# Optimization experiments

Measured on AMD Instinct MI355X. Metric: run time of the kernel, lower is better.

Reference implementation:

```python
import jax, jax.numpy as jnp
import numpy as np

B, L, D = 2, 4096, 768   # batch, seq_len, in_dim
BN = 384                 # bottleneck = in_dim / reduction_rate(2)
DI = 768                 # d_inner = expand(2) * bottleneck
NS = 16                  # d_state
DC = 4                   # d_conv
R  = 24                  # dt_rank = ceil(bottleneck / 16)


def _ln(x, g, b):
    m = x.mean(-1, keepdims=True)
    v = ((x - m) ** 2).mean(-1, keepdims=True)
    return (x - m) / jnp.sqrt(v + 1e-5) * g + b


def _mamba(x, in_W, conv_w, conv_b, xproj_W, dt_W, dt_b, A_log, Dp, out_W):
    # x: (B, L, BN)
    Bb, Ll, _ = x.shape
    xz = x @ in_W                                  # (B, L, 2*DI)
    xs, z = jnp.split(xz, 2, axis=-1)
    # causal depthwise conv over time
    xc = jnp.transpose(xs, (0, 2, 1))              # (B, DI, L)
    xc = jax.lax.conv_general_dilated(
        xc, conv_w[:, None, :], (1,), [(DC - 1, 0)],
        dimension_numbers=('NCH', 'OIH', 'NCH'), feature_group_count=DI)
    xc = jax.nn.silu(xc + conv_b[None, :, None])
    u = jnp.transpose(xc, (0, 2, 1))               # (B, L, DI)
    x_dbl = u @ xproj_W                            # (B, L, R + 2*NS)
    dt, Bm, Cm = jnp.split(x_dbl, [R, R + NS], axis=-1)
    dt = jax.nn.softplus(dt @ dt_W + dt_b)         # (B, L, DI)
    A = -jnp.exp(A_log)                            # (DI, NS)

    def step(h, inp):
        dt_t, B_t, C_t, u_t = inp                  # (B,DI),(B,NS),(B,NS),(B,DI)
        dA = jnp.exp(dt_t[:, :, None] * A)         # (B, DI, NS)
        h = dA * h + (dt_t * u_t)[:, :, None] * B_t[:, None, :]
        y = (h * C_t[:, None, :]).sum(-1)          # (B, DI)
        return h, y

    tm = lambda a: jnp.transpose(a, (1, 0, 2))     # time-major
    h0 = jnp.zeros((Bb, DI, NS), x.dtype)
    _, ys = jax.lax.scan(step, h0, (tm(dt), tm(Bm), tm(Cm), tm(u)))
    y = jnp.transpose(ys, (1, 0, 2)) + u * Dp      # (B, L, DI)
    y = y * jax.nn.silu(z)
    return y @ out_W                               # (B, L, BN)


def setup_inputs() -> dict:
    key = jax.random.key(0)
    ks = jax.random.split(key, 32)
    n = lambda i, shape, s=0.02: jax.random.normal(ks[i], shape, jnp.float32) * s
    inp = {
        'x': jax.random.normal(ks[0], (B, L, D), jnp.float32),
        'down_W': n(1, (D, BN)), 'down_b': jnp.zeros((BN,), jnp.float32),
        'up_W': n(2, (BN, D)), 'up_b': jnp.zeros((D,), jnp.float32),
    }
    A_log = jnp.log(jnp.tile(jnp.arange(1, NS + 1, dtype=jnp.float32), (DI, 1)))
    for pi, p in enumerate(['f', 'b']):
        o = 3 + pi * 10
        inp[p + '_in_W'] = n(o, (BN, 2 * DI))
        inp[p + '_conv_w'] = n(o + 1, (DI, DC), 0.1)
        inp[p + '_conv_b'] = jnp.zeros((DI,), jnp.float32)
        inp[p + '_xproj_W'] = n(o + 2, (DI, R + 2 * NS))
        inp[p + '_dt_W'] = n(o + 3, (R, DI), 0.1)
        inp[p + '_dt_b'] = n(o + 4, (DI,), 0.5)
        inp[p + '_A_log'] = A_log
        inp[p + '_D'] = jnp.ones((DI,), jnp.float32)
        inp[p + '_out_W'] = n(o + 5, (DI, BN))
        inp[p + '_ln_g'] = jnp.ones((BN,), jnp.float32)
        inp[p + '_ln_b'] = jnp.zeros((BN,), jnp.float32)
    return inp


def reference(x, down_W, down_b, up_W, up_b,
              f_in_W, f_conv_w, f_conv_b, f_xproj_W, f_dt_W, f_dt_b, f_A_log, f_D, f_out_W, f_ln_g, f_ln_b,
              b_in_W, b_conv_w, b_conv_b, b_xproj_W, b_dt_W, b_dt_b, b_A_log, b_D, b_out_W, b_ln_g, b_ln_b):
    h = x @ down_W + down_b                        # (B, L, BN)
    fwd = _ln(_mamba(h, f_in_W, f_conv_w, f_conv_b, f_xproj_W, f_dt_W, f_dt_b,
                     f_A_log, f_D, f_out_W), f_ln_g, f_ln_b)
    bwd = _ln(_mamba(h[:, ::-1], b_in_W, b_conv_w, b_conv_b, b_xproj_W, b_dt_W, b_dt_b,
                     b_A_log, b_D, b_out_W), b_ln_g, b_ln_b)
    y = fwd + bwd[:, ::-1]
    return y @ up_W + up_b
```

## Files before the change

### kernel.cpp

```cpp
#include <hip/hip_runtime.h>

typedef short bf16x8 __attribute__((ext_vector_type(8)));
typedef float f32x4 __attribute__((ext_vector_type(4)));
typedef float f32x2 __attribute__((ext_vector_type(2)));
typedef unsigned int u32x4 __attribute__((ext_vector_type(4)));

constexpr int Bq  = 2;
constexpr int Lq  = 4096;
constexpr int BNq = 384;
constexpr int DIq = 768;
constexpr int NSq = 16;
constexpr int Rq  = 24;
constexpr int XDq = 56;
constexpr int XLD = 64;
constexpr int CSq = 32;
constexpr int NCq = Lq / CSq;

__device__ __forceinline__ float b2f(unsigned short u) {
    unsigned int x = ((unsigned int)u) << 16;
    return __builtin_bit_cast(float, x);
}
__device__ __forceinline__ unsigned short f2b(float f) {
    unsigned int x = __builtin_bit_cast(unsigned int, f);
    return (unsigned short)((x + 0x8000u) >> 16);
}
__device__ __forceinline__ f32x2 bfpair(unsigned int v) {
    f32x2 r;
    r[0] = __builtin_bit_cast(float, v << 16);
    r[1] = __builtin_bit_cast(float, v & 0xFFFF0000u);
    return r;
}
__device__ __forceinline__ float softplus_fast(float v) {
    float e = __expf(-fabsf(v));
    return fmaxf(v, 0.f) + __logf(1.f + e);
}

typedef const __attribute__((address_space(1))) void gvoid_t;
typedef __attribute__((address_space(3))) void svoid_t;
__device__ __forceinline__ void gload_lds16(const void* g, void* l) {
    __builtin_amdgcn_global_load_lds((gvoid_t*)g, (svoid_t*)l, 16, 0, 0);
}

__device__ __forceinline__ void vm_wait(int n) {
    if (n <= 0)      asm volatile("s_waitcnt vmcnt(0)" ::: "memory");
    else if (n == 1) asm volatile("s_waitcnt vmcnt(1)" ::: "memory");
    else if (n == 2) asm volatile("s_waitcnt vmcnt(2)" ::: "memory");
    else if (n == 3) asm volatile("s_waitcnt vmcnt(3)" ::: "memory");
    else if (n == 4) asm volatile("s_waitcnt vmcnt(4)" ::: "memory");
    else if (n == 5) asm volatile("s_waitcnt vmcnt(5)" ::: "memory");
    else if (n == 6) asm volatile("s_waitcnt vmcnt(6)" ::: "memory");
    else if (n == 7) asm volatile("s_waitcnt vmcnt(6)" ::: "memory");
    else             asm volatile("s_waitcnt vmcnt(8)" ::: "memory");
}

__global__ __launch_bounds__(256) void cast_k(
    const float* __restrict__ src, unsigned short* __restrict__ dst, int n4)
{
    int i = blockIdx.x * 256 + threadIdx.x;
    if (i >= n4) return;
    f32x4 v = *(const f32x4*)(src + (size_t)i * 4);
    unsigned short o[4];
#pragma unroll
    for (int k = 0; k < 4; ++k) o[k] = f2b(v[k]);
    *(unsigned long long*)(dst + (size_t)i * 4) = *(unsigned long long*)o;
}

template<int BM, int BN, int WM, int WN, int TM, int TN, int NBUF, bool SWZ = false, int MINW = 2>
__global__ __launch_bounds__(WM * WN * 64, MINW) void gemm_t(
    const unsigned short* __restrict__ Ag, int lda, long sA,
    const unsigned short* __restrict__ Wg, long sW,
    const float* __restrict__ bias0, const float* __restrict__ bias1,
    void* __restrict__ Cg, int ldc, long sC,
    int Nn, int Kk, int epi)
{
    constexpr int NW   = WM * WN;
    constexpr int HALF = (BM + BN) * 32;
    constexpr int RT   = TM * 16;
    constexpr int CT   = TN * 16;
    constexpr int EPSH = RT * CT;
    constexpr int SMSZ = (NBUF * HALF > NW * EPSH) ? NBUF * HALF : NW * EPSH;
    __shared__ __align__(16) unsigned short Sm[SMSZ];

    const int z = blockIdx.z;
    const unsigned short* A = Ag + (size_t)z * sA;
    const unsigned short* W = Wg + (size_t)z * sW;
    const float* bias = z ? bias1 : bias0;

    int bx = blockIdx.x, by = blockIdx.y;
    if (SWZ) {
        int gx = gridDim.x, gy = gridDim.y;
        int stripe = bx & 7;
        int idx = (bx >> 3) + (gx >> 3) * by;
        int lin = stripe * ((gx >> 3) * gy) + idx;
        bx = lin / gy; by = lin % gy;
    }
    const int m0   = bx * BM;
    const int n0   = by * BN;

    const int tid  = threadIdx.x;
    const int lane = tid & 63;
    const int wid  = tid >> 6;
    const int row0 = (wid % WM) * RT;
    const int col0 = (wid / WM) * CT;
    const int lrow = lane & 15;
    const int lq   = lane >> 4;
    const int sub  = lane & 15;
    const int q    = lane >> 4;

    constexpr int NRG = (BM + BN) / 16;
    static_assert(NRG % NW == 0, "need uniform loads per wave for vmcnt counting");
    constexpr int NG = NRG / NW;
    constexpr int D  = NBUF - 1;

    const unsigned short* gbase[NG];
    {
        int ng = 0;
        for (int rg = wid; rg < NRG; rg += NW, ++ng) {
            if (rg * 16 < BM) gbase[ng] = A + (size_t)(m0 + rg * 16 + sub) * lda + q * 8;
            else              gbase[ng] = W + (size_t)(n0 + (rg * 16 - BM) + sub) * Kk + q * 8;
        }
    }
    auto stage = [&](int buf, int k0) {
        int ng = 0;
        for (int rg = wid; rg < NRG; rg += NW, ++ng)
            gload_lds16(gbase[ng] + k0, &Sm[buf * HALF + rg * 512]);
    };

    f32x4 zero4 = {0.f, 0.f, 0.f, 0.f};
    f32x4 acc[TM][TN];
#pragma unroll
    for (int i = 0; i < TM; ++i)
#pragma unroll
        for (int j = 0; j < TN; ++j) acc[i][j] = zero4;

    const int nsteps = Kk >> 5;
    for (int i = 0; i < D && i < nsteps; ++i) stage(i, i * 32);

    int buf = 0;
    for (int k = 0; k < nsteps; ++k) {
        int rem = nsteps - (k + 1);
        vm_wait((rem < D - 1 ? rem : D - 1) * NG);
        __builtin_amdgcn_s_barrier();
        asm volatile("" ::: "memory");

        if (k + D < nsteps) {
            int wb = buf + D; if (wb >= NBUF) wb -= NBUF;
            stage(wb, (k + D) * 32);
        }

        const unsigned short* As = &Sm[buf * HALF];
        const unsigned short* Bs = As + BM * 32;
        bf16x8 af[TM], bfv[TN];
#pragma unroll
        for (int i = 0; i < TM; ++i)
            af[i] = *(const bf16x8*)(&As[((row0 >> 4) + i) * 512 + lq * 128 + lrow * 8]);
#pragma unroll
        for (int j = 0; j < TN; ++j)
            bfv[j] = *(const bf16x8*)(&Bs[((col0 >> 4) + j) * 512 + lq * 128 + lrow * 8]);
#pragma unroll
        for (int i = 0; i < TM; ++i)
#pragma unroll
            for (int j = 0; j < TN; ++j)
                acc[i][j] = __builtin_amdgcn_mfma_f32_16x16x32_bf16(af[i], bfv[j], acc[i][j], 0, 0, 0);
        if (++buf == NBUF) buf = 0;
    }

    if (epi == 3) {
#pragma unroll
        for (int j = 0; j < TN; ++j) {
            int col = n0 + col0 + j * 16 + lrow;
            if (col >= Nn) continue;
            float bv = bias ? bias[col] : 0.f;
#pragma unroll
            for (int i = 0; i < TM; ++i)
#pragma unroll
                for (int r = 0; r < 4; ++r) {
                    int rowm = m0 + row0 + i * 16 + lq * 4 + r;
                    ((float*)Cg)[(size_t)z * sC + (size_t)rowm * ldc + col] = acc[i][j][r] + bv;
                }
        }
    } else {
        __syncthreads();
        unsigned short* Ep = Sm + wid * EPSH;
#pragma unroll
        for (int j = 0; j < TN; ++j) {
            int col = n0 + col0 + j * 16 + lrow;
            float bv = bias ? bias[col] : 0.f;
#pragma unroll
            for (int i = 0; i < TM; ++i)
#pragma unroll
                for (int r = 0; r < 4; ++r) {
                    float v = acc[i][j][r] + bv;
                    if (epi == 2) v = softplus_fast(v);
                    Ep[(i * 16 + lq * 4 + r) * CT + j * 16 + lrow] = f2b(v);
                }
        }
#pragma unroll
        for (int e = 0; e < EPSH / 512; ++e) {
            int ei = e * 512 + lane * 8;
            int lr = ei / CT, lc = ei % CT;
            int gr = m0 + row0 + lr, gc = n0 + col0 + lc;
            if (gc < Nn) {
                bf16x8 v = *(const bf16x8*)(&Ep[lr * CT + lc]);
                *(bf16x8*)((unsigned short*)Cg + (size_t)z * sC + (size_t)gr * ldc + gc) = v;
            }
        }
    }
}

__global__ __launch_bounds__(256) void conv_silu_k(
    const unsigned short* __restrict__ xz,
    const float* __restrict__ cwf, const float* __restrict__ cbf,
    const float* __restrict__ cwb, const float* __restrict__ cbb,
    unsigned short* __restrict__ u)
{
    int idx = blockIdx.x * 256 + threadIdx.x;
    int dir = blockIdx.y;
    int row = idx / 96;
    int c   = (idx - row * 96) * 8;
    int bb = row >> 12, tt = row & (Lq - 1);

    const float* cw = dir ? cwb : cwf;
    const float* cb = dir ? cbb : cbf;

    f32x4 w[8];
#pragma unroll
    for (int e = 0; e < 8; ++e) w[e] = *(const f32x4*)(cw + (c + e) * 4);
    f32x4 b0 = *(const f32x4*)(cb + c);
    f32x4 b1 = *(const f32x4*)(cb + c + 4);

    float acc[8];
#pragma unroll
    for (int e = 0; e < 4; ++e) { acc[e] = b0[e]; acc[4 + e] = b1[e]; }

#pragma unroll
    for (int j = 0; j < 4; ++j) {
        int ts = dir ? (tt + j) : (tt - 3 + j);
        int widx = dir ? (3 - j) : j;
        if (ts >= 0 && ts < Lq) {
            bf16x8 xv = *(const bf16x8*)(xz + (size_t)((bb << 12) + ts) * 3072 + dir * 1536 + c);
#pragma unroll
            for (int e = 0; e < 8; ++e)
                acc[e] += w[e][widx] * b2f(((unsigned short*)&xv)[e]);
        }
    }

    unsigned short o[8];
#pragma unroll
    for (int e = 0; e < 8; ++e) {
        float s = acc[e] / (1.f + __expf(-acc[e]));
        o[e] = f2b(s);
    }
    *(bf16x8*)(u + ((size_t)dir * 8192 + row) * DIq + c) = *(bf16x8*)o;
}

__device__ __forceinline__ void gp_ladder(float g1, f32x2 (&gp2)[8]) {
    float g2 = g1 * g1;
    gp2[0][0] = g1; gp2[0][1] = g2;
    f32x2 e2; e2[0] = g2; e2[1] = g2;
    gp2[1] = gp2[0] * e2;
    f32x2 e4; e4[0] = gp2[1][1]; e4[1] = gp2[1][1];
    gp2[2] = gp2[0] * e4;
    gp2[3] = gp2[1] * e4;
    f32x2 e8; e8[0] = gp2[3][1]; e8[1] = gp2[3][1];
#pragma unroll
    for (int k = 0; k < 4; ++k) gp2[4 + k] = gp2[k] * e8;
}

template<int DIR>
__device__ __forceinline__ void scan_p1_impl(
    const unsigned short* __restrict__ dt,
    const unsigned short* __restrict__ u,
    const unsigned short* __restrict__ xdbl,
    float* __restrict__ S, float* __restrict__ sumdt,
    int chunk, int cb3, int bb)
{
    const int ch = cb3 * 256 + threadIdx.x;
    const size_t rowbase = (size_t)DIR * 8192 + (bb << 12) + chunk * CSq;

    constexpr int sgn = DIR ? -1 : 1;
    constexpr int tt0 = DIR ? (CSq - 1) : 0;
    constexpr int PF  = 4;
    constexpr int NGR = CSq / PF;
    static_assert(CSq % PF == 0, "pf");

    const unsigned short* pd = dt + (rowbase + tt0) * DIq + ch;
    const unsigned short* pu = u  + (rowbase + tt0) * DIq + ch;
    const u32x4* prow = (const u32x4*)(xdbl + (rowbase + tt0) * XLD + Rq);

    f32x2 h2[8];
#pragma unroll
    for (int k = 0; k < 8; ++k) { h2[k][0] = 0.f; h2[k][1] = 0.f; }
    float sdt = 0.f;

    unsigned short db_[PF], ub_[PF];
#pragma unroll
    for (int i = 0; i < PF; ++i) {
        db_[i] = *pd; ub_[i] = *pu;
        pd += sgn * DIq; pu += sgn * DIq;
    }
    u32x4 q0 = prow[0], q1 = prow[1];

    auto body = [&](unsigned short dv16, unsigned short uv16,
                    const u32x4& a0, const u32x4& a1) {
        float dtv = b2f(dv16);
        float uv  = b2f(uv16);
        float du  = dtv * uv;
        sdt += dtv;
        f32x2 du2; du2[0] = du; du2[1] = du;
        f32x2 gp2[8];
        gp_ladder(__expf(-dtv), gp2);
        unsigned int w[8] = {a0[0], a0[1], a0[2], a0[3], a1[0], a1[1], a1[2], a1[3]};
#pragma unroll
        for (int k = 0; k < 8; ++k)
            h2[k] = h2[k] * gp2[k] + du2 * bfpair(w[k]);
    };

#pragma unroll 1
    for (int g = 0; g < NGR - 1; ++g) {
#pragma unroll
        for (int i = 0; i < PF; ++i) {
            unsigned short dv = db_[i], uv = ub_[i];
            db_[i] = *pd; ub_[i] = *pu;
            pd += sgn * DIq; pu += sgn * DIq;
            prow += sgn * 8;
            u32x4 n0 = prow[0], n1 = prow[1];
            body(dv, uv, q0, q1);
            q0 = n0; q1 = n1;
        }
    }
#pragma unroll
    for (int i = 0; i < PF; ++i) {
        unsigned short dv = db_[i], uv = ub_[i];
        if (i < PF - 1) {
            prow += sgn * 8;
            u32x4 n0 = prow[0], n1 = prow[1];
            body(dv, uv, q0, q1);
            q0 = n0; q1 = n1;
        } else {
            body(dv, uv, q0, q1);
        }
    }

    size_t base = (((size_t)DIR * Bq + bb) * NCq + chunk) * DIq + ch;
    sumdt[base] = sdt;
    f32x4* Sp = (f32x4*)(S + base * 16);
#pragma unroll
    for (int q4 = 0; q4 < 4; ++q4) {
        f32x4 t;
        t[0] = h2[2 * q4][0]; t[1] = h2[2 * q4][1];
        t[2] = h2[2 * q4 + 1][0]; t[3] = h2[2 * q4 + 1][1];
        Sp[q4] = t;
    }
}

__global__ __launch_bounds__(256) void scan_p1_k(
    const unsigned short* __restrict__ dt,
    const unsigned short* __restrict__ u,
    const unsigned short* __restrict__ xdbl,
    float* __restrict__ S, float* __restrict__ sumdt)
{
    int dir = blockIdx.z >> 1, bb = blockIdx.z & 1;
    if (dir == 0) scan_p1_impl<0>(dt, u, xdbl, S, sumdt, blockIdx.x, blockIdx.y, bb);
    else          scan_p1_impl<1>(dt, u, xdbl, S, sumdt, blockIdx.x, blockIdx.y, bb);
}

__global__ __launch_bounds__(256) void scan_p2_k(
    const float* __restrict__ sumdt,
    float* __restrict__ S)
{
    int idx = blockIdx.x * 256 + threadIdx.x;
    int ss = idx & 15;
    int rest = idx >> 4;
    int ch = rest % DIq;
    int db = rest / DIq;
    int dir = db >> 1;
    float Av = -(float)(ss + 1);

    constexpr int TB = 16;
    constexpr int NT = NCq / TB;
    static_assert(NCq % TB == 0, "tile");

    auto baseOf = [&](int i) {
        int c = dir ? (NCq - 1 - i) : i;
        return ((size_t)db * NCq + c) * DIq + ch;
    };

    float svA[TB], sdA[TB], svB[TB], sdB[TB];

    auto loadT = [&](int t, float (&sv)[TB], float (&sd)[TB]) {
#pragma unroll
        for (int i = 0; i < TB; ++i) {
            size_t b = baseOf(t * TB + i);
            sv[i] = S[b * 16 + ss];
            sd[i] = sumdt[b];
        }
    };

    float h = 0.f;
    auto chainT = [&](int t, const float (&sv)[TB], const float (&sd)[TB]) {
#pragma unroll
        for (int i = 0; i < TB; ++i) {
            size_t b = baseOf(t * TB + i);
            S[b * 16 + ss] = h;
            h = h * __expf(Av * sd[i]) + sv[i];
        }
    };

    loadT(0, svA, sdA);
#pragma unroll
    for (int t = 0; t < NT; t += 2) {
        if (t + 1 < NT) loadT(t + 1, svB, sdB);
        chainT(t, svA, sdA);
        if (t + 2 < NT) loadT(t + 2, svA, sdA);
        if (t + 1 < NT) chainT(t + 1, svB, sdB);
    }
}

template<int DIR>
__device__ __forceinline__ void scan_p3_impl(
    const unsigned short* __restrict__ dt,
    const unsigned short* __restrict__ u,
    const unsigned short* __restrict__ xdbl,
    unsigned short* __restrict__ xz,
    const float* __restrict__ Dp,
    const float* __restrict__ Hin,
    int chunk, int cb3, int bb)
{
    const int ch = cb3 * 256 + threadIdx.x;
    const size_t rowbase = (size_t)DIR * 8192 + (bb << 12) + chunk * CSq;
    const float Dv = Dp[ch];

    constexpr int sgn = DIR ? -1 : 1;
    constexpr int tt0 = DIR ? (CSq - 1) : 0;
    constexpr int PF  = 4;
    constexpr int NGR = CSq / PF;
    static_assert(CSq % PF == 0, "pf");
    const size_t lbase = (size_t)(bb << 12) + chunk * CSq;

    const unsigned short* pd = dt + (rowbase + tt0) * DIq + ch;
    const unsigned short* pu = u  + (rowbase + tt0) * DIq + ch;
    const unsigned short* pz = xz + (lbase + tt0) * 3072 + DIR * 1536 + 768 + ch;
    unsigned short*       py = xz + (lbase + tt0) * 3072 + DIR * 1536 + ch;
    const u32x4* prow = (const u32x4*)(xdbl + (rowbase + tt0) * XLD + Rq);

    unsigned short db_[PF], ub_[PF], zb_[PF];
#pragma unroll
    for (int i = 0; i < PF; ++i) {
        db_[i] = *pd; ub_[i] = *pu; zb_[i] = *pz;
        pd += sgn * DIq; pu += sgn * DIq; pz += (long)sgn * 3072;
    }

    size_t base = (((size_t)DIR * Bq + bb) * NCq + chunk) * DIq + ch;
    f32x2 h2[8];
    {
        const f32x4* Hp = (const f32x4*)(Hin + base * 16);
#pragma unroll
        for (int q4 = 0; q4 < 4; ++q4) {
            f32x4 t = Hp[q4];
            h2[2 * q4][0] = t[0]; h2[2 * q4][1] = t[1];
            h2[2 * q4 + 1][0] = t[2]; h2[2 * q4 + 1][1] = t[3];
        }
    }

    u32x4 q0 = prow[0], q1 = prow[1], q2 = prow[2], q3 = prow[3];

    auto body = [&](unsigned short dv16, unsigned short uv16, unsigned short zv16,
                    const u32x4& a0, const u32x4& a1,
                    const u32x4& c0, const u32x4& c1) {
        float dtv = b2f(dv16);
        float uv  = b2f(uv16);
        float du  = dtv * uv;
        f32x2 du2; du2[0] = du; du2[1] = du;
        f32x2 gp2[8];
        gp_ladder(__expf(-dtv), gp2);
        unsigned int wb[8] = {a0[0], a0[1], a0[2], a0[3], a1[0], a1[1], a1[2], a1[3]};
        unsigned int wc[8] = {c0[0], c0[1], c0[2], c0[3], c1[0], c1[1], c1[2], c1[3]};
        f32x2 ya; ya[0] = 0.f; ya[1] = 0.f;
        f32x2 yb; yb[0] = 0.f; yb[1] = 0.f;
#pragma unroll
        for (int k = 0; k < 8; ++k) {
            h2[k] = h2[k] * gp2[k] + du2 * bfpair(wb[k]);
            if (k & 1) yb = yb + h2[k] * bfpair(wc[k]);
            else       ya = ya + h2[k] * bfpair(wc[k]);
        }
        f32x2 yt = ya + yb;
        float y = yt[0] + yt[1];
        float zv = b2f(zv16);
        float yv = (y + uv * Dv) * (zv / (1.f + __expf(-zv)));
        *py = f2b(yv);
    };

#pragma unroll 1
    for (int g = 0; g < NGR - 1; ++g) {
#pragma unroll
        for (int i = 0; i < PF; ++i) {
            unsigned short dv = db_[i], uv = ub_[i], zv = zb_[i];
            db_[i] = *pd; ub_[i] = *pu; zb_[i] = *pz;
            pd += sgn * DIq; pu += sgn * DIq; pz += (long)sgn * 3072;
            prow += sgn * 8;
            u32x4 n0 = prow[0], n1 = prow[1], n2 = prow[2], n3 = prow[3];
            body(dv, uv, zv, q0, q1, q2, q3);
            py += (long)sgn * 3072;
            q0 = n0; q1 = n1; q2 = n2; q3 = n3;
        }
    }
#pragma unroll
    for (int i = 0; i < PF; ++i) {
        unsigned short dv = db_[i], uv = ub_[i], zv = zb_[i];
        if (i < PF - 1) {
            prow += sgn * 8;
            u32x4 n0 = prow[0], n1 = prow[1], n2 = prow[2], n3 = prow[3];
            body(dv, uv, zv, q0, q1, q2, q3);
            py += (long)sgn * 3072;
            q0 = n0; q1 = n1; q2 = n2; q3 = n3;
        } else {
            body(dv, uv, zv, q0, q1, q2, q3);
        }
    }
}

__global__ __launch_bounds__(256) void scan_p3_k(
    const unsigned short* __restrict__ dt,
    const unsigned short* __restrict__ u,
    const unsigned short* __restrict__ xdbl,
    unsigned short* __restrict__ xz,
    const float* __restrict__ Dp0, const float* __restrict__ Dp1,
    const float* __restrict__ Hin)
{
    int dir = blockIdx.z >> 1, bb = blockIdx.z & 1;
    if (dir == 0) scan_p3_impl<0>(dt, u, xdbl, xz, Dp0, Hin, blockIdx.x, blockIdx.y, bb);
    else          scan_p3_impl<1>(dt, u, xdbl, xz, Dp1, Hin, blockIdx.x, blockIdx.y, bb);
}

__global__ __launch_bounds__(256) void ln_add_k(
    const unsigned short* __restrict__ xin,
    const float* __restrict__ g0, const float* __restrict__ b0,
    const float* __restrict__ g1, const float* __restrict__ b1,
    unsigned short* __restrict__ out)
{
    int wid = threadIdx.x >> 6, lane = threadIdx.x & 63;
    size_t row = blockIdx.x * 4 + wid;
    const size_t half = (size_t)8192 * BNq;
    const unsigned short* xf = xin + row * BNq;
    const unsigned short* xb = xin + half + row * BNq;

    float vf[6], vb[6];
#pragma unroll
    for (int i = 0; i < 6; ++i) { vf[i] = b2f(xf[lane + i * 64]); vb[i] = b2f(xb[lane + i * 64]); }

    float sf = 0.f, sb = 0.f;
#pragma unroll
    for (int i = 0; i < 6; ++i) { sf += vf[i]; sb += vb[i]; }
#pragma unroll
    for (int off = 32; off > 0; off >>= 1) { sf += __shfl_down(sf, off, 64); sb += __shfl_down(sb, off, 64); }
    sf = __shfl(sf, 0, 64); sb = __shfl(sb, 0, 64);
    float mf = sf / 384.f, mb = sb / 384.f;

    float qf = 0.f, qb = 0.f;
#pragma unroll
    for (int i = 0; i < 6; ++i) {
        float df = vf[i] - mf; qf += df * df;
        float db = vb[i] - mb; qb += db * db;
    }
#pragma unroll
    for (int off = 32; off > 0; off >>= 1) { qf += __shfl_down(qf, off, 64); qb += __shfl_down(qb, off, 64); }
    qf = __shfl(qf, 0, 64); qb = __shfl(qb, 0, 64);
    float invf = rsqrtf(qf / 384.f + 1e-5f);
    float invb = rsqrtf(qb / 384.f + 1e-5f);

    unsigned short* orow = out + row * BNq;
#pragma unroll
    for (int i = 0; i < 6; ++i) {
        int c = lane + i * 64;
        float a = (vf[i] - mf) * invf * g0[c] + b0[c];
        float b = (vb[i] - mb) * invb * g1[c] + b1[c];
        orow[c] = f2b(a + b);
    }
}

struct TDesc { const float* src; unsigned short* dst; int R, C, Rp, Cp; };
struct TPack { TDesc d[10]; };

__global__ __launch_bounds__(256) void transpose_all_k(TPack p)
{
    TDesc t = p.d[blockIdx.z];
    int c0 = blockIdx.x * 32, r0 = blockIdx.y * 32;
    if (c0 >= t.Cp || r0 >= t.Rp) return;
    __shared__ float tile[32][33];
    int tx = threadIdx.x & 31, ty = threadIdx.x >> 5;
#pragma unroll
    for (int i = 0; i < 4; ++i) {
        int r = r0 + ty + i * 8;
        float v = 0.f;
        if (r < t.R && (c0 + tx) < t.C) v = t.src[(size_t)r * t.C + c0 + tx];
        tile[ty + i * 8][tx] = v;
    }
    __syncthreads();
#pragma unroll
    for (int i = 0; i < 4; ++i) {
        int c = c0 + ty + i * 8;
        if (c < t.Cp && (r0 + tx) < t.Rp)
            t.dst[(size_t)c * t.Rp + r0 + tx] = f2b(tile[tx][ty + i * 8]);
    }
}

extern "C" void kernel_launch(void* const* d_in, const int* in_sizes, int n_in,
                              void* d_out, int out_size, void* d_ws, size_t ws_size,
                              hipStream_t stream)
{
    (void)in_sizes; (void)n_in; (void)out_size; (void)ws_size;
    auto inf = [&](int i) { return (const float*)d_in[i]; };

    const float* Xin   = inf(0);
    const float* downW = inf(1);
    const float* downB = inf(2);
    const float* upW   = inf(3);
    const float* upB   = inf(4);

    char* ws = (char*)d_ws;
    size_t off = 0;
    auto alloc = [&](size_t bytes) -> char* {
        char* p = ws + off;
        off += (bytes + 255) & ~(size_t)255;
        return p;
    };
    unsigned short* Xb     = (unsigned short*)alloc((size_t)8192 * 768 * 2);
    unsigned short* WT_down= (unsigned short*)alloc(384 * 768 * 2);
    unsigned short* WT_up  = (unsigned short*)alloc(768 * 384 * 2);
    unsigned short* WT_in  = (unsigned short*)alloc((size_t)3072 * 384 * 2);
    unsigned short* WT_xp  = (unsigned short*)alloc((size_t)2 * 64 * 768 * 2);
    unsigned short* WT_dt  = (unsigned short*)alloc((size_t)2 * 768 * 32 * 2);
    unsigned short* WT_out = (unsigned short*)alloc((size_t)2 * 384 * 768 * 2);
    unsigned short* hbuf   = (unsigned short*)alloc((size_t)8192 * 384 * 2);
    unsigned short* xzbuf  = (unsigned short*)alloc((size_t)8192 * 3072 * 2);
    unsigned short* ubuf   = (unsigned short*)alloc((size_t)2 * 8192 * 768 * 2);
    unsigned short* xdbl   = (unsigned short*)alloc((size_t)2 * 8192 * XLD * 2);
    unsigned short* dtbuf  = (unsigned short*)alloc((size_t)2 * 8192 * 768 * 2);
    float* Sbuf  = (float*)alloc((size_t)2 * Bq * NCq * 768 * 16 * 4);
    float* sumdt = (float*)alloc((size_t)2 * Bq * NCq * 768 * 4);

    unsigned short* ysum   = Xb;
    unsigned short* tmp384 = dtbuf;

    cast_k<<<dim3(8192 * 768 / 4 / 256), 256, 0, stream>>>(Xin, Xb, 8192 * 768 / 4);

    TPack tp;
    tp.d[0] = {downW, WT_down, 768, 384, 768, 384};
    tp.d[1] = {upW,   WT_up,   384, 768, 384, 768};
    for (int d = 0; d < 2; ++d) {
        int o = 5 + d * 11;
        tp.d[2 + d * 4] = {inf(o + 0), WT_in + (size_t)d * 1536 * 384, 384, 1536, 384, 1536};
        tp.d[3 + d * 4] = {inf(o + 3), WT_xp + (size_t)d * 64 * 768,   768, 56,   768, 64};
        tp.d[4 + d * 4] = {inf(o + 4), WT_dt + (size_t)d * 768 * 32,   24,  768,  32,  768};
        tp.d[5 + d * 4] = {inf(o + 8), WT_out + (size_t)d * 384 * 768, 768, 384,  768, 384};
    }
    transpose_all_k<<<dim3(48, 24, 10), 256, 0, stream>>>(tp);

    gemm_t<64,64,2,2,2,2,4,true><<<dim3(128, 6), 256, 0, stream>>>(
        Xb, 768, 0, WT_down, 0, downB, downB, hbuf, 384, 0, 384, 768, 1);

    gemm_t<128,256,2,4,4,4,3,true,4><<<dim3(64, 12), 512, 0, stream>>>(
        hbuf, 384, 0, WT_in, 0, nullptr, nullptr, xzbuf, 3072, 0, 3072, 384, 0);

    conv_silu_k<<<dim3(3072, 2), 256, 0, stream>>>(
        xzbuf, inf(6), inf(7), inf(17), inf(18), ubuf);

    gemm_t<64,64,2,2,2,2,4><<<dim3(128, 1, 2), 256, 0, stream>>>(
        ubuf, 768, (long)8192 * 768, WT_xp, (long)64 * 768,
        nullptr, nullptr, xdbl, XLD, (long)8192 * XLD, XDq, 768, 0);

    gemm_t<64,64,2,2,2,2,4><<<dim3(128, 12, 2), 256, 0, stream>>>(
        xdbl, XLD, (long)8192 * XLD, WT_dt, (long)768 * 32,
        inf(10), inf(21), dtbuf, 768, (long)8192 * 768, 768, 32, 2);

    scan_p1_k<<<dim3(NCq, 3, 4), 256, 0, stream>>>(dtbuf, ubuf, xdbl, Sbuf, sumdt);
    scan_p2_k<<<dim3(192), 256, 0, stream>>>(sumdt, Sbuf);
    scan_p3_k<<<dim3(NCq, 3, 4), 256, 0, stream>>>(
        dtbuf, ubuf, xdbl, xzbuf, inf(12), inf(23), Sbuf);

    gemm_t<64,64,2,2,2,2,4><<<dim3(128, 6, 2), 256, 0, stream>>>(
        xzbuf, 3072, (long)1536, WT_out, (long)384 * 768,
        nullptr, nullptr, tmp384, 384, (long)8192 * 384, 384, 768, 0);

    ln_add_k<<<dim3(2048), 256, 0, stream>>>(
        tmp384, inf(14), inf(15), inf(25), inf(26), ysum);

    gemm_t<64,64,2,2,2,2,4,true><<<dim3(128, 12), 256, 0, stream>>>(
        ysum, 384, 0, WT_up, 0, upB, upB, (float*)d_out, 768, 0, 768, 384, 3);
}
```

Before: 379.0 us.

## Store chunk scan states in fp16, prefetch decay exp, raise scan occupancy

```diff
diff --git a/kernel.cpp b/kernel.cpp
--- a/kernel.cpp
+++ b/kernel.cpp
@@ -1,4 +1,5 @@
 #include <hip/hip_runtime.h>
+#include <hip/hip_fp16.h>
 
 typedef short bf16x8 __attribute__((ext_vector_type(8)));
 typedef float f32x4 __attribute__((ext_vector_type(4)));
@@ -24,6 +25,12 @@
     unsigned int x = __builtin_bit_cast(unsigned int, f);
     return (unsigned short)((x + 0x8000u) >> 16);
 }
+__device__ __forceinline__ float h2f_(unsigned short h) {
+    return __half2float(__builtin_bit_cast(__half, h));
+}
+__device__ __forceinline__ unsigned short f2h_(float f) {
+    return __builtin_bit_cast(unsigned short, __float2half(f));
+}
 __device__ __forceinline__ f32x2 bfpair(unsigned int v) {
     f32x2 r;
     r[0] = __builtin_bit_cast(float, v << 16);
@@ -272,7 +279,7 @@
     const unsigned short* __restrict__ dt,
     const unsigned short* __restrict__ u,
     const unsigned short* __restrict__ xdbl,
-    float* __restrict__ S, float* __restrict__ sumdt,
+    unsigned short* __restrict__ S, float* __restrict__ sumdt,
     int chunk, int cb3, int bb)
 {
     const int ch = cb3 * 256 + threadIdx.x;
@@ -300,8 +307,9 @@
         pd += sgn * DIq; pu += sgn * DIq;
     }
     u32x4 q0 = prow[0], q1 = prow[1];
-
-    auto body = [&](unsigned short dv16, unsigned short uv16,
+    float g1cur = __expf(-b2f(db_[0]));
+
+    auto body = [&](unsigned short dv16, unsigned short uv16, float g1,
                     const u32x4& a0, const u32x4& a1) {
         float dtv = b2f(dv16);
         float uv  = b2f(uv16);
@@ -309,7 +317,7 @@
         sdt += dtv;
         f32x2 du2; du2[0] = du; du2[1] = du;
         f32x2 gp2[8];
-        gp_ladder(__expf(-dtv), gp2);
+        gp_ladder(g1, gp2);
         unsigned int w[8] = {a0[0], a0[1], a0[2], a0[3], a1[0], a1[1], a1[2], a1[3]};
 #pragma unroll
         for (int k = 0; k < 8; ++k)
@@ -325,7 +333,10 @@
             pd += sgn * DIq; pu += sgn * DIq;
             prow += sgn * 8;
             u32x4 n0 = prow[0], n1 = prow[1];
-            body(dv, uv, q0, q1);
+            unsigned short dnxt = (i < PF - 1) ? db_[i + 1] : db_[0];
+            float g1n = __expf(-b2f(dnxt));
+            body(dv, uv, g1cur, q0, q1);
+            g1cur = g1n;
             q0 = n0; q1 = n1;
         }
     }
@@ -333,32 +344,35 @@
     for (int i = 0; i < PF; ++i) {
         unsigned short dv = db_[i], uv = ub_[i];
         if (i < PF - 1) {
+            float g1n = __expf(-b2f(db_[i + 1]));
             prow += sgn * 8;
             u32x4 n0 = prow[0], n1 = prow[1];
-            body(dv, uv, q0, q1);
+            body(dv, uv, g1cur, q0, q1);
+            g1cur = g1n;
             q0 = n0; q1 = n1;
         } else {
-            body(dv, uv, q0, q1);
+            body(dv, uv, g1cur, q0, q1);
         }
     }
 
     size_t base = (((size_t)DIR * Bq + bb) * NCq + chunk) * DIq + ch;
     sumdt[base] = sdt;
-    f32x4* Sp = (f32x4*)(S + base * 16);
-#pragma unroll
-    for (int q4 = 0; q4 < 4; ++q4) {
-        f32x4 t;
-        t[0] = h2[2 * q4][0]; t[1] = h2[2 * q4][1];
-        t[2] = h2[2 * q4 + 1][0]; t[3] = h2[2 * q4 + 1][1];
-        Sp[q4] = t;
-    }
-}
-
-__global__ __launch_bounds__(256) void scan_p1_k(
+    unsigned short o16[16];
+#pragma unroll
+    for (int k = 0; k < 8; ++k) {
+        o16[2 * k]     = f2h_(h2[k][0]);
+        o16[2 * k + 1] = f2h_(h2[k][1]);
+    }
+    bf16x8* Sp = (bf16x8*)(S + base * 16);
+    Sp[0] = ((bf16x8*)o16)[0];
+    Sp[1] = ((bf16x8*)o16)[1];
+}
+
+__global__ __launch_bounds__(256, 8) void scan_p1_k(
     const unsigned short* __restrict__ dt,
     const unsigned short* __restrict__ u,
     const unsigned short* __restrict__ xdbl,
-    float* __restrict__ S, float* __restrict__ sumdt)
+    unsigned short* __restrict__ S, float* __restrict__ sumdt)
 {
     int dir = blockIdx.z >> 1, bb = blockIdx.z & 1;
     if (dir == 0) scan_p1_impl<0>(dt, u, xdbl, S, sumdt, blockIdx.x, blockIdx.y, bb);
@@ -367,7 +381,7 @@
 
 __global__ __launch_bounds__(256) void scan_p2_k(
     const float* __restrict__ sumdt,
-    float* __restrict__ S)
+    unsigned short* __restrict__ S)
 {
     int idx = blockIdx.x * 256 + threadIdx.x;
     int ss = idx & 15;
@@ -392,7 +406,7 @@
 #pragma unroll
         for (int i = 0; i < TB; ++i) {
             size_t b = baseOf(t * TB + i);
-            sv[i] = S[b * 16 + ss];
+            sv[i] = h2f_(S[b * 16 + ss]);
             sd[i] = sumdt[b];
         }
     };
@@ -402,7 +416,7 @@
 #pragma unroll
         for (int i = 0; i < TB; ++i) {
             size_t b = baseOf(t * TB + i);
-            S[b * 16 + ss] = h;
+            S[b * 16 + ss] = f2h_(h);
             h = h * __expf(Av * sd[i]) + sv[i];
         }
     };
@@ -424,7 +438,7 @@
     const unsigned short* __restrict__ xdbl,
     unsigned short* __restrict__ xz,
     const float* __restrict__ Dp,
-    const float* __restrict__ Hin,
+    const unsigned short* __restrict__ Hin,
     int chunk, int cb3, int bb)
 {
     const int ch = cb3 * 256 + threadIdx.x;
@@ -454,18 +468,22 @@
     size_t base = (((size_t)DIR * Bq + bb) * NCq + chunk) * DIq + ch;
     f32x2 h2[8];
     {
-        const f32x4* Hp = (const f32x4*)(Hin + base * 16);
-#pragma unroll
-        for (int q4 = 0; q4 < 4; ++q4) {
-            f32x4 t = Hp[q4];
-            h2[2 * q4][0] = t[0]; h2[2 * q4][1] = t[1];
-            h2[2 * q4 + 1][0] = t[2]; h2[2 * q4 + 1][1] = t[3];
+        const bf16x8* Hp = (const bf16x8*)(Hin + base * 16);
+        bf16x8 t0 = Hp[0], t1 = Hp[1];
+#pragma unroll
+        for (int k = 0; k < 4; ++k) {
+            h2[k][0] = h2f_(((unsigned short*)&t0)[2 * k]);
+            h2[k][1] = h2f_(((unsigned short*)&t0)[2 * k + 1]);
+            h2[4 + k][0] = h2f_(((unsigned short*)&t1)[2 * k]);
+            h2[4 + k][1] = h2f_(((unsigned short*)&t1)[2 * k + 1]);
         }
     }
 
     u32x4 q0 = prow[0], q1 = prow[1], q2 = prow[2], q3 = prow[3];
+    float g1cur = __expf(-b2f(db_[0]));
 
     auto body = [&](unsigned short dv16, unsigned short uv16, unsigned short zv16,
+                    float g1,
                     const u32x4& a0, const u32x4& a1,
                     const u32x4& c0, const u32x4& c1) {
         float dtv = b2f(dv16);
@@ -473,7 +491,7 @@
         float du  = dtv * uv;
         f32x2 du2; du2[0] = du; du2[1] = du;
         f32x2 gp2[8];
-        gp_ladder(__expf(-dtv), gp2);
+        gp_ladder(g1, gp2);
         unsigned int wb[8] = {a0[0], a0[1], a0[2], a0[3], a1[0], a1[1], a1[2], a1[3]};
         unsigned int wc[8] = {c0[0], c0[1], c0[2], c0[3], c1[0], c1[1], c1[2], c1[3]};
         f32x2 ya; ya[0] = 0.f; ya[1] = 0.f;
@@ -500,7 +518,10 @@
             pd += sgn * DIq; pu += sgn * DIq; pz += (long)sgn * 3072;
             prow += sgn * 8;
             u32x4 n0 = prow[0], n1 = prow[1], n2 = prow[2], n3 = prow[3];
-            body(dv, uv, zv, q0, q1, q2, q3);
+            unsigned short dnxt = (i < PF - 1) ? db_[i + 1] : db_[0];
+            float g1n = __expf(-b2f(dnxt));
+            body(dv, uv, zv, g1cur, q0, q1, q2, q3);
+            g1cur = g1n;
             py += (long)sgn * 3072;
             q0 = n0; q1 = n1; q2 = n2; q3 = n3;
         }
@@ -509,24 +530,26 @@
     for (int i = 0; i < PF; ++i) {
         unsigned short dv = db_[i], uv = ub_[i], zv = zb_[i];
         if (i < PF - 1) {
+            float g1n = __expf(-b2f(db_[i + 1]));
             prow += sgn * 8;
             u32x4 n0 = prow[0], n1 = prow[1], n2 = prow[2], n3 = prow[3];
-            body(dv, uv, zv, q0, q1, q2, q3);
+            body(dv, uv, zv, g1cur, q0, q1, q2, q3);
+            g1cur = g1n;
             py += (long)sgn * 3072;
             q0 = n0; q1 = n1; q2 = n2; q3 = n3;
         } else {
-            body(dv, uv, zv, q0, q1, q2, q3);
-        }
-    }
-}
-
-__global__ __launch_bounds__(256) void scan_p3_k(
+            body(dv, uv, zv, g1cur, q0, q1, q2, q3);
+        }
+    }
+}
+
+__global__ __launch_bounds__(256, 8) void scan_p3_k(
     const unsigned short* __restrict__ dt,
     const unsigned short* __restrict__ u,
     const unsigned short* __restrict__ xdbl,
     unsigned short* __restrict__ xz,
     const float* __restrict__ Dp0, const float* __restrict__ Dp1,
-    const float* __restrict__ Hin)
+    const unsigned short* __restrict__ Hin)
 {
     int dir = blockIdx.z >> 1, bb = blockIdx.z & 1;
     if (dir == 0) scan_p3_impl<0>(dt, u, xdbl, xz, Dp0, Hin, blockIdx.x, blockIdx.y, bb);
@@ -637,7 +660,7 @@
     unsigned short* ubuf   = (unsigned short*)alloc((size_t)2 * 8192 * 768 * 2);
     unsigned short* xdbl   = (unsigned short*)alloc((size_t)2 * 8192 * XLD * 2);
     unsigned short* dtbuf  = (unsigned short*)alloc((size_t)2 * 8192 * 768 * 2);
-    float* Sbuf  = (float*)alloc((size_t)2 * Bq * NCq * 768 * 16 * 4);
+    unsigned short* Sbuf   = (unsigned short*)alloc((size_t)2 * Bq * NCq * 768 * 16 * 2);
     float* sumdt = (float*)alloc((size_t)2 * Bq * NCq * 768 * 4);
 
     unsigned short* ysum   = Xb;
```

Measured after the change: 374.5 us. About the same (-1.2%).
